# Kernel tuning notes

Hardware: AMD Instinct MI355X
Metric: run time of the kernel (lower is better)

Reference implementation:

```python
import jax, jax.numpy as jnp
import numpy as np

DELTA_V = 0.5
DELTA_D = 3.0
PARAM_VAR = 1.0
PARAM_DIST = 1.0
PARAM_REG = 0.001
NUM_BIN_LABELS = 2   # binary labels in {0,1}
NUM_INST_LABELS = 6  # background + 5 lanes


def _disc_loss_single(pred, labels, num_labels, delta_v, delta_d):
    """pred: [D, N] float, labels: [N] int in [0, num_labels).
    Assumes all labels present (true w.h.p. for large N), so
    torch.unique(sorted=True) == arange(num_labels)."""
    D, N = pred.shape
    K = num_labels
    labels = labels.astype(jnp.int32)
    ones = jnp.ones((N,), dtype=pred.dtype)
    counts = jax.ops.segment_sum(ones, labels, num_segments=K)            # [K]
    sums = jax.ops.segment_sum(pred.T, labels, num_segments=K)            # [K, D]
    means = sums / counts[:, None]                                        # [K, D] segment means

    # variance (pull) term: distance of each pixel embedding to its segment mean
    mu_expand = means[labels]                                             # [N, D]
    dist = jnp.sqrt(jnp.sum((mu_expand - pred.T) ** 2, axis=1))           # [N]
    dist = jnp.maximum(dist - delta_v, 0.0) ** 2
    var_per_label = jax.ops.segment_sum(dist, labels, num_segments=K) / counts
    l_var = jnp.mean(var_per_label)

    # distance (push) term over all ordered pairs i != j of segment means
    diff = means[:, None, :] - means[None, :, :]                          # [K, K, D]
    sq = jnp.sum(diff ** 2, axis=-1)                                      # [K, K]
    offdiag = ~jnp.eye(K, dtype=bool)
    sq_safe = jnp.where(offdiag, sq, 1.0)  # avoid sqrt(0) grad NaN on diagonal
    dn = jnp.maximum(2.0 * delta_d - jnp.sqrt(sq_safe), 0.0) ** 2
    l_dist = jnp.sum(jnp.where(offdiag, dn, 0.0)) / (K * (K - 1))

    # regularizer: mean L2 norm of segment means (norm over feature dim)
    l_reg = jnp.mean(jnp.sqrt(jnp.sum(means ** 2, axis=1)))

    return PARAM_VAR * l_var + PARAM_DIST * l_dist + PARAM_REG * l_reg


def setup_inputs() -> dict:
    key = jax.random.key(0)
    k1, k2, k3, k4 = jax.random.split(key, 4)
    B, MN = 4, 512 * 1024
    return {
        "binary_logits": jax.random.normal(k1, (B, 2, MN), dtype=jnp.float32),
        "binary_labels": jax.random.randint(k2, (B, MN), 0, NUM_BIN_LABELS, dtype=jnp.int64),
        "instance_logits": jax.random.normal(k3, (B, 5, MN), dtype=jnp.float32),
        "instance_labels": jax.random.randint(k4, (B, MN), 0, NUM_INST_LABELS, dtype=jnp.int64),
    }


def reference(binary_logits, binary_labels, instance_logits, instance_labels):
    bin_loss_per = jax.vmap(
        lambda p, l: _disc_loss_single(p, l, NUM_BIN_LABELS, DELTA_V, DELTA_D)
    )(binary_logits, binary_labels)
    inst_loss_per = jax.vmap(
        lambda p, l: _disc_loss_single(p, l, NUM_INST_LABELS, DELTA_V, DELTA_D)
    )(instance_logits, instance_labels)
    return jnp.mean(bin_loss_per), jnp.mean(inst_loss_per)
```

## Files before the change

kernel.cpp:

```cpp
#include <hip/hip_runtime.h>
#include <math.h>

#define DELTA_V 0.5f
#define DELTA_D 3.0f
#define P_REG   0.001f

#define BPS   128
#define TPB   256
#define NVMAX 36

#define P1_OFF   0
#define CNT_OFF  (8 * BPS * 36)
#define MEAN_OFF (CNT_OFF + 48)
#define LDR_OFF  (MEAN_OFF + 240)
#define P2_OFF   (LDR_OFF + 8)

template<int K, int D>
__device__ void pass1_body(const float* __restrict__ pred,
                           const int*  __restrict__ labels,
                           float* __restrict__ partials,
                           int n4, float (*lredW)[NVMAX]) {
    constexpr int NV = K * (D + 1);
    const float4* pred4 = (const float4*)pred;
    const int4*   lab4  = (const int4*)labels;

    float acc[K][D + 1];
    #pragma unroll
    for (int k = 0; k < K; ++k)
        #pragma unroll
        for (int j = 0; j <= D; ++j) acc[k][j] = 0.f;

    const int idx0   = blockIdx.x * TPB + threadIdx.x;
    const int stride = BPS * TPB;
    for (int i = idx0; i < n4; i += stride) {
        int4 lv = lab4[i];
        int labs[4] = {lv.x, lv.y, lv.z, lv.w};
        float4 xv[D];
        #pragma unroll
        for (int d = 0; d < D; ++d) xv[d] = pred4[(size_t)d * n4 + i];
        const float* xs = (const float*)&xv[0];
        #pragma unroll
        for (int c = 0; c < 4; ++c) {
            const int lab = labs[c];
            #pragma unroll
            for (int k = 0; k < K; ++k) {
                const float ind = (lab == k) ? 1.f : 0.f;
                acc[k][D] += ind;
                #pragma unroll
                for (int d = 0; d < D; ++d)
                    acc[k][d] = fmaf(ind, xs[d * 4 + c], acc[k][d]);
            }
        }
    }

    const int wave = threadIdx.x >> 6, lane = threadIdx.x & 63;
    #pragma unroll
    for (int k = 0; k < K; ++k) {
        #pragma unroll
        for (int j = 0; j <= D; ++j) {
            float v = acc[k][j];
            for (int off = 32; off > 0; off >>= 1) v += __shfl_down(v, off);
            if (lane == 0) lredW[wave][k * (D + 1) + j] = v;
        }
    }
    __syncthreads();
    if (threadIdx.x < NV) {
        const int t = threadIdx.x;
        partials[t] = lredW[0][t] + lredW[1][t] + lredW[2][t] + lredW[3][t];
    }
}

__global__ __launch_bounds__(TPB)
void pass1_fused(const float* __restrict__ bl, const int* __restrict__ bL,
                 const float* __restrict__ il, const int* __restrict__ iL,
                 float* __restrict__ ws, int MN) {
    const int s = blockIdx.y, b = s & 3;
    __shared__ float lredW[4][NVMAX];
    float* partials = ws + P1_OFF + (size_t)(s * BPS + blockIdx.x) * NVMAX;
    if (s < 4) pass1_body<2, 2>(bl + (size_t)b * 2 * MN, bL + (size_t)b * MN, partials, MN >> 2, lredW);
    else       pass1_body<6, 5>(il + (size_t)b * 5 * MN, iL + (size_t)b * MN, partials, MN >> 2, lredW);
}

__global__ void mid_kernel(float* __restrict__ ws) {
    const int s = blockIdx.x;
    const int isInst = s >> 2;
    const int K = isInst ? 6 : 2, D = isInst ? 5 : 2;
    const int NV = K * (D + 1);
    const float* P = ws + P1_OFF + (size_t)s * BPS * NVMAX;
    const int t = threadIdx.x;
    __shared__ float tot[NVMAX];
    __shared__ float muS[30];
    __shared__ float cntS[6];
    if (t < NV) {
        float v = 0.f;
        for (int j = 0; j < BPS; ++j) v += P[j * NVMAX + t];
        tot[t] = v;
        const int k = t / (D + 1), jj = t % (D + 1);
        if (jj == D) { cntS[k] = v; ws[CNT_OFF + s * 6 + k] = v; }
    }
    __syncthreads();
    if (t < NV) {
        const int k = t / (D + 1), jj = t % (D + 1);
        if (jj < D) {
            const float m = tot[t] / cntS[k];
            muS[k * D + jj] = m;
            ws[MEAN_OFF + s * 30 + k * D + jj] = m;
        }
    }
    __syncthreads();
    if (t == 0) {
        float l_dist = 0.f, l_reg = 0.f;
        for (int i = 0; i < K; ++i) {
            float n2 = 0.f;
            for (int d = 0; d < D; ++d) n2 += muS[i * D + d] * muS[i * D + d];
            l_reg += sqrtf(n2);
            for (int j = 0; j < K; ++j) {
                if (i == j) continue;
                float sq = 0.f;
                for (int d = 0; d < D; ++d) { const float df = muS[i * D + d] - muS[j * D + d]; sq += df * df; }
                const float dn = fmaxf(2.f * DELTA_D - sqrtf(sq), 0.f);
                l_dist += dn * dn;
            }
        }
        l_dist /= (float)(K * (K - 1));
        l_reg  /= (float)K;
        ws[LDR_OFF + s] = l_dist + P_REG * l_reg;
    }
}

template<int K, int D>
__device__ void pass2_body(const float* __restrict__ pred,
                           const int*  __restrict__ labels,
                           const float* __restrict__ means,
                           float* __restrict__ partials,
                           int n4, float* mu, float (*lredW)[6]) {
    if (threadIdx.x < K * D) mu[threadIdx.x] = means[threadIdx.x];
    __syncthreads();

    const float4* pred4 = (const float4*)pred;
    const int4*   lab4  = (const int4*)labels;

    float acc[K];
    #pragma unroll
    for (int k = 0; k < K; ++k) acc[k] = 0.f;

    const int idx0   = blockIdx.x * TPB + threadIdx.x;
    const int stride = BPS * TPB;
    for (int i = idx0; i < n4; i += stride) {
        int4 lv = lab4[i];
        int labs[4] = {lv.x, lv.y, lv.z, lv.w};
        float4 xv[D];
        #pragma unroll
        for (int d = 0; d < D; ++d) xv[d] = pred4[(size_t)d * n4 + i];
        const float* xs = (const float*)&xv[0];
        #pragma unroll
        for (int c = 0; c < 4; ++c) {
            const int lab = labs[c];
            float sq = 0.f;
            #pragma unroll
            for (int d = 0; d < D; ++d) {
                const float df = mu[lab * D + d] - xs[d * 4 + c];
                sq = fmaf(df, df, sq);
            }
            const float h = fmaxf(sqrtf(sq) - DELTA_V, 0.f);
            const float h2 = h * h;
            #pragma unroll
            for (int k = 0; k < K; ++k)
                acc[k] += (lab == k) ? h2 : 0.f;
        }
    }

    const int wave = threadIdx.x >> 6, lane = threadIdx.x & 63;
    #pragma unroll
    for (int k = 0; k < K; ++k) {
        float v = acc[k];
        for (int off = 32; off > 0; off >>= 1) v += __shfl_down(v, off);
        if (lane == 0) lredW[wave][k] = v;
    }
    __syncthreads();
    if (threadIdx.x < K) {
        const int t = threadIdx.x;
        partials[t] = lredW[0][t] + lredW[1][t] + lredW[2][t] + lredW[3][t];
    }
}

__global__ __launch_bounds__(TPB)
void pass2_fused(const float* __restrict__ bl, const int* __restrict__ bL,
                 const float* __restrict__ il, const int* __restrict__ iL,
                 float* __restrict__ ws, int MN) {
    const int s = blockIdx.y, b = s & 3;
    __shared__ float mu[30];
    __shared__ float lredW[4][6];
    const float* means = ws + MEAN_OFF + s * 30;
    float* partials = ws + P2_OFF + (size_t)(s * BPS + blockIdx.x) * 6;
    if (s < 4) pass2_body<2, 2>(bl + (size_t)b * 2 * MN, bL + (size_t)b * MN, means, partials, MN >> 2, mu, lredW);
    else       pass2_body<6, 5>(il + (size_t)b * 5 * MN, iL + (size_t)b * MN, means, partials, MN >> 2, mu, lredW);
}

__global__ void final_kernel(const float* __restrict__ ws, float* __restrict__ out) {
    __shared__ float contrib[48];
    const int t = threadIdx.x;
    if (t < 48) {
        const int s = t / 6, k = t % 6;
        const int Ks = (s < 4) ? 2 : 6;
        float c = 0.f;
        if (k < Ks) {
            float v = 0.f;
            for (int j = 0; j < BPS; ++j) v += ws[P2_OFF + (size_t)(s * BPS + j) * 6 + k];
            c = v / ws[CNT_OFF + s * 6 + k];
        }
        contrib[t] = c;
    }
    __syncthreads();
    if (t == 0) {
        float totB = 0.f, totI = 0.f;
        for (int s = 0; s < 8; ++s) {
            const int Ks = (s < 4) ? 2 : 6;
            float lv = 0.f;
            for (int k = 0; k < Ks; ++k) lv += contrib[s * 6 + k];
            lv /= (float)Ks;
            const float loss = lv + ws[LDR_OFF + s];
            if (s < 4) totB += loss; else totI += loss;
        }
        out[0] = totB * 0.25f;
        out[1] = totI * 0.25f;
    }
}

extern "C" void kernel_launch(void* const* d_in, const int* in_sizes, int n_in,
                              void* d_out, int out_size, void* d_ws, size_t ws_size,
                              hipStream_t stream) {
    const float* bin_logits  = (const float*)d_in[0];
    const int*   bin_labels  = (const int*)d_in[1];
    const float* inst_logits = (const float*)d_in[2];
    const int*   inst_labels = (const int*)d_in[3];
    float* ws  = (float*)d_ws;
    float* out = (float*)d_out;

    const int B  = 4;
    const int MN = in_sizes[1] / B;

    dim3 grid(BPS, 8), block(TPB);
    pass1_fused<<<grid, block, 0, stream>>>(bin_logits, bin_labels, inst_logits, inst_labels, ws, MN);
    mid_kernel<<<8, 64, 0, stream>>>(ws);
    pass2_fused<<<grid, block, 0, stream>>>(bin_logits, bin_labels, inst_logits, inst_labels, ws, MN);
    final_kernel<<<1, 64, 0, stream>>>(ws, out);
}
```

Measured before the change: 141.0 us.

## Fuse all passes into one cooperative kernel keeping inputs in registers

```diff
diff --git a/kernel.cpp b/kernel.cpp
--- a/kernel.cpp
+++ b/kernel.cpp
@@ -1,16 +1,259 @@
 #include <hip/hip_runtime.h>
+#include <hip/hip_cooperative_groups.h>
 #include <math.h>
+
+namespace cg = cooperative_groups;
 
 #define DELTA_V 0.5f
 #define DELTA_D 3.0f
 #define P_REG   0.001f
-
-#define BPS   128
-#define TPB   256
-#define NVMAX 36
-
+#define TPB     256
+#define NVMAX   36
+
+typedef float f32x4 __attribute__((ext_vector_type(4)));
+typedef int   i32x4 __attribute__((ext_vector_type(4)));
+
+#define BPSB 64
+#define BPSI 128
+#define NBLK (4 * BPSB + 4 * BPSI)
+
+#define FP1_OFF   0
+#define FCNT_OFF  (NBLK * NVMAX)
+#define FMEAN_OFF (FCNT_OFF + 48)
+#define FLDR_OFF  (FMEAN_OFF + 240)
+#define FP2_OFF   (FLDR_OFF + 8)
+
+__device__ __forceinline__ int slice_block_base(int s) {
+    return (s < 4) ? s * BPSB : 4 * BPSB + (s - 4) * BPSI;
+}
+
+template<int K, int D, int NBP>
+__device__ void reduce_means(const float* __restrict__ ws, int sliceBase,
+                             float* cntS, float* muS) {
+    constexpr int NV = K * (D + 1);
+    constexpr int G  = TPB / NV;
+    __shared__ float red[TPB];
+    __shared__ float tot[NVMAX];
+    const int t = threadIdx.x;
+    if (t < G * NV) {
+        const int g = t / NV, v = t - g * NV;
+        float sm = 0.f;
+        for (int j = g; j < NBP; j += G)
+            sm += ws[FP1_OFF + (size_t)(sliceBase + j) * NVMAX + v];
+        red[t] = sm;
+    }
+    __syncthreads();
+    if (t < NV) {
+        float sm = 0.f;
+        #pragma unroll
+        for (int g = 0; g < G; ++g) sm += red[g * NV + t];
+        tot[t] = sm;
+        const int k = t / (D + 1), jj = t - k * (D + 1);
+        if (jj == D) cntS[k] = sm;
+    }
+    __syncthreads();
+    if (t < NV) {
+        const int k = t / (D + 1), jj = t - k * (D + 1);
+        if (jj < D) muS[k * D + jj] = tot[t] / cntS[k];
+    }
+    __syncthreads();
+}
+
+__device__ void final_body(const float* __restrict__ ws, float* __restrict__ out) {
+    __shared__ float contrib[48];
+    const int t = threadIdx.x;
+    if (t < 48) {
+        const int s = t / 6, k = t - s * 6;
+        const int Ks = (s < 4) ? 2 : 6;
+        const int NB = (s < 4) ? BPSB : BPSI;
+        const int base = slice_block_base(s);
+        float c = 0.f;
+        if (k < Ks) {
+            float v = 0.f;
+            for (int j = 0; j < NB; ++j)
+                v += ws[FP2_OFF + (size_t)(base + j) * 6 + k];
+            c = v / ws[FCNT_OFF + s * 6 + k];
+        }
+        contrib[t] = c;
+    }
+    __syncthreads();
+    if (t == 0) {
+        float totB = 0.f, totI = 0.f;
+        for (int s = 0; s < 8; ++s) {
+            const int Ks = (s < 4) ? 2 : 6;
+            float lv = 0.f;
+            for (int k = 0; k < Ks; ++k) lv += contrib[s * 6 + k];
+            lv /= (float)Ks;
+            const float loss = lv + ws[FLDR_OFF + s];
+            if (s < 4) totB += loss; else totI += loss;
+        }
+        out[0] = totB * 0.25f;
+        out[1] = totI * 0.25f;
+    }
+}
+
+template<int K, int D, int NITER, int NBP>
+__device__ void run_slice(const float* __restrict__ pred, const int* __restrict__ labels,
+                          float* __restrict__ ws, float* __restrict__ out,
+                          const int s, const int bx, const int bid, const int n4) {
+    constexpr int NV = K * (D + 1);
+    const f32x4* __restrict__ pred4 = (const f32x4*)pred;
+    const i32x4* __restrict__ lab4  = (const i32x4*)labels;
+
+    __shared__ float lredW[4][NVMAX];
+    __shared__ float cntS[6];
+    __shared__ float muS[30];
+
+    f32x4 xv[NITER][D];
+    int   lp[NITER];
+
+    const int idx0 = bx * TPB + threadIdx.x;
+    const f32x4 zero4 = {0.f, 0.f, 0.f, 0.f};
+
+    #pragma unroll
+    for (int it = 0; it < NITER; ++it) {
+        const int i = idx0 + it * (NBP * TPB);
+        if (i < n4) {
+            const i32x4 l4 = lab4[i];
+            lp[it] = l4[0] | (l4[1] << 8) | (l4[2] << 16) | (l4[3] << 24);
+            #pragma unroll
+            for (int d = 0; d < D; ++d) xv[it][d] = pred4[(size_t)d * n4 + i];
+        } else {
+            lp[it] = -1;
+            #pragma unroll
+            for (int d = 0; d < D; ++d) xv[it][d] = zero4;
+        }
+    }
+
+    float acc[K][D + 1];
+    #pragma unroll
+    for (int k = 0; k < K; ++k) {
+        #pragma unroll
+        for (int j = 0; j <= D; ++j) acc[k][j] = 0.f;
+    }
+    #pragma unroll
+    for (int it = 0; it < NITER; ++it) {
+        #pragma unroll
+        for (int c = 0; c < 4; ++c) {
+            const int lab = (lp[it] >> (8 * c)) & 0xFF;
+            #pragma unroll
+            for (int k = 0; k < K; ++k) {
+                const float ind = (lab == k) ? 1.f : 0.f;
+                acc[k][D] += ind;
+                #pragma unroll
+                for (int d = 0; d < D; ++d)
+                    acc[k][d] = fmaf(ind, xv[it][d][c], acc[k][d]);
+            }
+        }
+    }
+
+    const int wave = threadIdx.x >> 6, lane = threadIdx.x & 63;
+    #pragma unroll
+    for (int k = 0; k < K; ++k) {
+        #pragma unroll
+        for (int j = 0; j <= D; ++j) {
+            float v = acc[k][j];
+            #pragma unroll
+            for (int off = 32; off; off >>= 1) v += __shfl_down(v, off);
+            if (lane == 0) lredW[wave][k * (D + 1) + j] = v;
+        }
+    }
+    __syncthreads();
+    if (threadIdx.x < NV)
+        ws[FP1_OFF + (size_t)bid * NVMAX + threadIdx.x] =
+            lredW[0][threadIdx.x] + lredW[1][threadIdx.x] +
+            lredW[2][threadIdx.x] + lredW[3][threadIdx.x];
+
+    cg::grid_group grid = cg::this_grid();
+    grid.sync();
+
+    reduce_means<K, D, NBP>(ws, bid - bx, cntS, muS);
+
+    if (bx == 0) {
+        const int t = threadIdx.x;
+        if (t < K) ws[FCNT_OFF + s * 6 + t] = cntS[t];
+        if (t < K * D) ws[FMEAN_OFF + s * 30 + t] = muS[t];
+        if (t == 0) {
+            float l_dist = 0.f, l_reg = 0.f;
+            for (int i = 0; i < K; ++i) {
+                float n2 = 0.f;
+                for (int d = 0; d < D; ++d) n2 += muS[i * D + d] * muS[i * D + d];
+                l_reg += sqrtf(n2);
+                for (int j = 0; j < K; ++j) {
+                    if (i == j) continue;
+                    float sq = 0.f;
+                    for (int d = 0; d < D; ++d) {
+                        const float df = muS[i * D + d] - muS[j * D + d];
+                        sq += df * df;
+                    }
+                    const float dn = fmaxf(2.f * DELTA_D - sqrtf(sq), 0.f);
+                    l_dist += dn * dn;
+                }
+            }
+            ws[FLDR_OFF + s] = l_dist / (float)(K * (K - 1)) + P_REG * (l_reg / (float)K);
+        }
+    }
+
+    float acc2[K];
+    #pragma unroll
+    for (int k = 0; k < K; ++k) acc2[k] = 0.f;
+    #pragma unroll
+    for (int it = 0; it < NITER; ++it) {
+        #pragma unroll
+        for (int c = 0; c < 4; ++c) {
+            const int lab = (lp[it] >> (8 * c)) & 0xFF;
+            const int lb  = (lab < K) ? lab : 0;
+            float sq = 0.f;
+            #pragma unroll
+            for (int d = 0; d < D; ++d) {
+                const float df = muS[lb * D + d] - xv[it][d][c];
+                sq = fmaf(df, df, sq);
+            }
+            const float h  = fmaxf(sqrtf(sq) - DELTA_V, 0.f);
+            const float h2 = h * h;
+            #pragma unroll
+            for (int k = 0; k < K; ++k) acc2[k] += (lab == k) ? h2 : 0.f;
+        }
+    }
+    #pragma unroll
+    for (int k = 0; k < K; ++k) {
+        float v = acc2[k];
+        #pragma unroll
+        for (int off = 32; off; off >>= 1) v += __shfl_down(v, off);
+        if (lane == 0) lredW[wave][k] = v;
+    }
+    __syncthreads();
+    if (threadIdx.x < K)
+        ws[FP2_OFF + (size_t)bid * 6 + threadIdx.x] =
+            lredW[0][threadIdx.x] + lredW[1][threadIdx.x] +
+            lredW[2][threadIdx.x] + lredW[3][threadIdx.x];
+
+    grid.sync();
+
+    if (bid == 0) final_body(ws, out);
+}
+
+__global__ __launch_bounds__(TPB, 3)
+void fused_kernel(const float* __restrict__ bl, const int* __restrict__ bL,
+                  const float* __restrict__ il, const int* __restrict__ iL,
+                  float* __restrict__ ws, float* __restrict__ out, int MN) {
+    const int bid = blockIdx.x;
+    const int n4  = MN >> 2;
+    if (bid < 4 * BPSB) {
+        const int s = bid / BPSB, bx = bid - s * BPSB;
+        run_slice<2, 2, 8, BPSB>(bl + (size_t)s * 2 * MN, bL + (size_t)s * MN,
+                                 ws, out, s, bx, bid, n4);
+    } else {
+        const int r = bid - 4 * BPSB;
+        const int si = r / BPSI, bx = r - si * BPSI;
+        run_slice<6, 5, 4, BPSI>(il + (size_t)si * 5 * MN, iL + (size_t)si * MN,
+                                 ws, out, 4 + si, bx, bid, n4);
+    }
+}
+
+#define OBPS 128
 #define P1_OFF   0
-#define CNT_OFF  (8 * BPS * 36)
+#define CNT_OFF  (8 * OBPS * 36)
 #define MEAN_OFF (CNT_OFF + 48)
 #define LDR_OFF  (MEAN_OFF + 240)
 #define P2_OFF   (LDR_OFF + 8)
@@ -26,19 +269,20 @@
 
     float acc[K][D + 1];
     #pragma unroll
-    for (int k = 0; k < K; ++k)
+    for (int k = 0; k < K; ++k) {
         #pragma unroll
         for (int j = 0; j <= D; ++j) acc[k][j] = 0.f;
+    }
 
     const int idx0   = blockIdx.x * TPB + threadIdx.x;
-    const int stride = BPS * TPB;
+    const int stride = OBPS * TPB;
     for (int i = idx0; i < n4; i += stride) {
         int4 lv = lab4[i];
         int labs[4] = {lv.x, lv.y, lv.z, lv.w};
-        float4 xv[D];
-        #pragma unroll
-        for (int d = 0; d < D; ++d) xv[d] = pred4[(size_t)d * n4 + i];
-        const float* xs = (const float*)&xv[0];
+        float4 xvv[D];
+        #pragma unroll
+        for (int d = 0; d < D; ++d) xvv[d] = pred4[(size_t)d * n4 + i];
+        const float* xs = (const float*)&xvv[0];
         #pragma unroll
         for (int c = 0; c < 4; ++c) {
             const int lab = labs[c];
@@ -76,7 +320,7 @@
                  float* __restrict__ ws, int MN) {
     const int s = blockIdx.y, b = s & 3;
     __shared__ float lredW[4][NVMAX];
-    float* partials = ws + P1_OFF + (size_t)(s * BPS + blockIdx.x) * NVMAX;
+    float* partials = ws + P1_OFF + (size_t)(s * OBPS + blockIdx.x) * NVMAX;
     if (s < 4) pass1_body<2, 2>(bl + (size_t)b * 2 * MN, bL + (size_t)b * MN, partials, MN >> 2, lredW);
     else       pass1_body<6, 5>(il + (size_t)b * 5 * MN, iL + (size_t)b * MN, partials, MN >> 2, lredW);
 }
@@ -86,14 +330,14 @@
     const int isInst = s >> 2;
     const int K = isInst ? 6 : 2, D = isInst ? 5 : 2;
     const int NV = K * (D + 1);
-    const float* P = ws + P1_OFF + (size_t)s * BPS * NVMAX;
+    const float* P = ws + P1_OFF + (size_t)s * OBPS * NVMAX;
     const int t = threadIdx.x;
     __shared__ float tot[NVMAX];
     __shared__ float muS[30];
     __shared__ float cntS[6];
     if (t < NV) {
         float v = 0.f;
-        for (int j = 0; j < BPS; ++j) v += P[j * NVMAX + t];
+        for (int j = 0; j < OBPS; ++j) v += P[j * NVMAX + t];
         tot[t] = v;
         const int k = t / (D + 1), jj = t % (D + 1);
         if (jj == D) { cntS[k] = v; ws[CNT_OFF + s * 6 + k] = v; }
@@ -145,14 +389,14 @@
     for (int k = 0; k < K; ++k) acc[k] = 0.f;
 
     const int idx0   = blockIdx.x * TPB + threadIdx.x;
-    const int stride = BPS * TPB;
+    const int stride = OBPS * TPB;
     for (int i = idx0; i < n4; i += stride) {
         int4 lv = lab4[i];
         int labs[4] = {lv.x, lv.y, lv.z, lv.w};
-        float4 xv[D];
-        #pragma unroll
-        for (int d = 0; d < D; ++d) xv[d] = pred4[(size_t)d * n4 + i];
-        const float* xs = (const float*)&xv[0];
+        float4 xvv[D];
+        #pragma unroll
+        for (int d = 0; d < D; ++d) xvv[d] = pred4[(size_t)d * n4 + i];
+        const float* xs = (const float*)&xvv[0];
         #pragma unroll
         for (int c = 0; c < 4; ++c) {
             const int lab = labs[c];
@@ -192,7 +436,7 @@
     __shared__ float mu[30];
     __shared__ float lredW[4][6];
     const float* means = ws + MEAN_OFF + s * 30;
-    float* partials = ws + P2_OFF + (size_t)(s * BPS + blockIdx.x) * 6;
+    float* partials = ws + P2_OFF + (size_t)(s * OBPS + blockIdx.x) * 6;
     if (s < 4) pass2_body<2, 2>(bl + (size_t)b * 2 * MN, bL + (size_t)b * MN, means, partials, MN >> 2, mu, lredW);
     else       pass2_body<6, 5>(il + (size_t)b * 5 * MN, iL + (size_t)b * MN, means, partials, MN >> 2, mu, lredW);
 }
@@ -206,7 +450,7 @@
         float c = 0.f;
         if (k < Ks) {
             float v = 0.f;
-            for (int j = 0; j < BPS; ++j) v += ws[P2_OFF + (size_t)(s * BPS + j) * 6 + k];
+            for (int j = 0; j < OBPS; ++j) v += ws[P2_OFF + (size_t)(s * OBPS + j) * 6 + k];
             c = v / ws[CNT_OFF + s * 6 + k];
         }
         contrib[t] = c;
@@ -230,19 +474,28 @@
 extern "C" void kernel_launch(void* const* d_in, const int* in_sizes, int n_in,
                               void* d_out, int out_size, void* d_ws, size_t ws_size,
                               hipStream_t stream) {
-    const float* bin_logits  = (const float*)d_in[0];
-    const int*   bin_labels  = (const int*)d_in[1];
-    const float* inst_logits = (const float*)d_in[2];
-    const int*   inst_labels = (const int*)d_in[3];
+    const float* bl = (const float*)d_in[0];
+    const int*   bL = (const int*)d_in[1];
+    const float* il = (const float*)d_in[2];
+    const int*   iL = (const int*)d_in[3];
     float* ws  = (float*)d_ws;
     float* out = (float*)d_out;
 
     const int B  = 4;
-    const int MN = in_sizes[1] / B;
-
-    dim3 grid(BPS, 8), block(TPB);
-    pass1_fused<<<grid, block, 0, stream>>>(bin_logits, bin_labels, inst_logits, inst_labels, ws, MN);
-    mid_kernel<<<8, 64, 0, stream>>>(ws);
-    pass2_fused<<<grid, block, 0, stream>>>(bin_logits, bin_labels, inst_logits, inst_labels, ws, MN);
-    final_kernel<<<1, 64, 0, stream>>>(ws, out);
-}
+    int MN = in_sizes[1] / B;
+
+    void* args[] = {(void*)&bl, (void*)&bL, (void*)&il, (void*)&iL,
+                    (void*)&ws, (void*)&out, (void*)&MN};
+    hipError_t err = hipLaunchCooperativeKernel(
+        reinterpret_cast<const void*>(&fused_kernel),
+        dim3(NBLK), dim3(TPB), args, 0u, stream);
+
+    if (err != hipSuccess) {
+        (void)hipGetLastError();
+        dim3 grid(OBPS, 8), block(TPB);
+        pass1_fused<<<grid, block, 0, stream>>>(bl, bL, il, iL, ws, MN);
+        mid_kernel<<<8, 64, 0, stream>>>(ws);
+        pass2_fused<<<grid, block, 0, stream>>>(bl, bL, il, iL, ws, MN);
+        final_kernel<<<1, 64, 0, stream>>>(ws, out);
+    }
+}
```

Result: slower. 269.3 us (+90.9%).

## Fold mid and final kernels into pass2, rebalance blocks toward instance slices

Applied to the files above, without the earlier changes.

```diff
diff --git a/kernel.cpp b/kernel.cpp
--- a/kernel.cpp
+++ b/kernel.cpp
@@ -4,22 +4,28 @@
 #define DELTA_V 0.5f
 #define DELTA_D 3.0f
 #define P_REG   0.001f
-
-#define BPS   128
-#define TPB   256
-#define NVMAX 36
-
-#define P1_OFF   0
-#define CNT_OFF  (8 * BPS * 36)
-#define MEAN_OFF (CNT_OFF + 48)
-#define LDR_OFF  (MEAN_OFF + 240)
-#define P2_OFF   (LDR_OFF + 8)
+#define TPB     256
+#define NVMAX   36
+
+#define BPSB 128
+#define BPSI 256
+#define NBLK (4 * BPSB + 4 * BPSI)
+
+#define CTR_OFF   0
+#define P1_OFF    16
+#define SCAL_OFF  (P1_OFF + NBLK * NVMAX)
+#define P2_OFF    (SCAL_OFF + 64)
+
+__device__ __forceinline__ int slice_base(int s) {
+    return (s < 4) ? s * BPSB : 4 * BPSB + (s - 4) * BPSI;
+}
 
 template<int K, int D>
 __device__ void pass1_body(const float* __restrict__ pred,
                            const int*  __restrict__ labels,
                            float* __restrict__ partials,
-                           int n4, float (*lredW)[NVMAX]) {
+                           int n4, int bx, int stride,
+                           float (*lredW)[NVMAX]) {
     constexpr int NV = K * (D + 1);
     const float4* pred4 = (const float4*)pred;
     const int4*   lab4  = (const int4*)labels;
@@ -30,8 +36,7 @@
         #pragma unroll
         for (int j = 0; j <= D; ++j) acc[k][j] = 0.f;
 
-    const int idx0   = blockIdx.x * TPB + threadIdx.x;
-    const int stride = BPS * TPB;
+    const int idx0 = bx * TPB + threadIdx.x;
     for (int i = idx0; i < n4; i += stride) {
         int4 lv = lab4[i];
         int labs[4] = {lv.x, lv.y, lv.z, lv.w};
@@ -71,71 +76,111 @@
 }
 
 __global__ __launch_bounds__(TPB)
-void pass1_fused(const float* __restrict__ bl, const int* __restrict__ bL,
-                 const float* __restrict__ il, const int* __restrict__ iL,
-                 float* __restrict__ ws, int MN) {
-    const int s = blockIdx.y, b = s & 3;
+void pass1_k(const float* __restrict__ bl, const int* __restrict__ bL,
+             const float* __restrict__ il, const int* __restrict__ iL,
+             float* __restrict__ ws, int MN) {
+    if (blockIdx.x == 0 && threadIdx.x == 0) ((int*)ws)[CTR_OFF] = 0;
+
     __shared__ float lredW[4][NVMAX];
-    float* partials = ws + P1_OFF + (size_t)(s * BPS + blockIdx.x) * NVMAX;
-    if (s < 4) pass1_body<2, 2>(bl + (size_t)b * 2 * MN, bL + (size_t)b * MN, partials, MN >> 2, lredW);
-    else       pass1_body<6, 5>(il + (size_t)b * 5 * MN, iL + (size_t)b * MN, partials, MN >> 2, lredW);
-}
-
-__global__ void mid_kernel(float* __restrict__ ws) {
-    const int s = blockIdx.x;
-    const int isInst = s >> 2;
-    const int K = isInst ? 6 : 2, D = isInst ? 5 : 2;
-    const int NV = K * (D + 1);
-    const float* P = ws + P1_OFF + (size_t)s * BPS * NVMAX;
+    const int bid = blockIdx.x, n4 = MN >> 2;
+    float* partials = ws + P1_OFF + (size_t)bid * NVMAX;
+    if (bid < 4 * BPSB) {
+        const int s = bid / BPSB, bx = bid - s * BPSB;
+        pass1_body<2, 2>(bl + (size_t)s * 2 * MN, bL + (size_t)s * MN,
+                         partials, n4, bx, BPSB * TPB, lredW);
+    } else {
+        const int r = bid - 4 * BPSB;
+        const int si = r / BPSI, bx = r - si * BPSI;
+        pass1_body<6, 5>(il + (size_t)si * 5 * MN, iL + (size_t)si * MN,
+                         partials, n4, bx, BPSI * TPB, lredW);
+    }
+}
+
+__device__ void final_body(const float* __restrict__ ws, float* __restrict__ out) {
+    __shared__ float contrib[48];
     const int t = threadIdx.x;
+    if (t < 48) {
+        const int s = t / 6, k = t - (t / 6) * 6;
+        const int Ks = (s < 4) ? 2 : 6;
+        const int NB = (s < 4) ? BPSB : BPSI;
+        const int base = slice_base(s);
+        float c = 0.f;
+        if (k < Ks) {
+            float v = 0.f;
+            for (int j = 0; j < NB; ++j)
+                v += ws[P2_OFF + (size_t)(base + j) * 6 + k];
+            c = v / ws[SCAL_OFF + s * 8 + k];
+        }
+        contrib[t] = c;
+    }
+    __syncthreads();
+    if (t == 0) {
+        float totB = 0.f, totI = 0.f;
+        for (int s = 0; s < 8; ++s) {
+            const int Ks = (s < 4) ? 2 : 6;
+            float lv = 0.f;
+            for (int k = 0; k < Ks; ++k) lv += contrib[s * 6 + k];
+            lv /= (float)Ks;
+            const float loss = lv + ws[SCAL_OFF + s * 8 + 6];
+            if (s < 4) totB += loss; else totI += loss;
+        }
+        out[0] = totB * 0.25f;
+        out[1] = totI * 0.25f;
+    }
+}
+
+template<int K, int D, int NBP>
+__device__ void pass2_slice(const float* __restrict__ pred,
+                            const int*  __restrict__ labels,
+                            float* __restrict__ ws, float* __restrict__ out,
+                            const int s, const int bx, const int bid, const int n4) {
+    constexpr int NV = K * (D + 1);
     __shared__ float tot[NVMAX];
     __shared__ float muS[30];
     __shared__ float cntS[6];
+    __shared__ float lredW[4][6];
+    __shared__ int lastFlag;
+    const int t = threadIdx.x;
+    const int sliceBase = bid - bx;
+
     if (t < NV) {
+        const float* P = ws + P1_OFF + (size_t)sliceBase * NVMAX + t;
         float v = 0.f;
-        for (int j = 0; j < BPS; ++j) v += P[j * NVMAX + t];
+        for (int j = 0; j < NBP; ++j) v += P[(size_t)j * NVMAX];
         tot[t] = v;
-        const int k = t / (D + 1), jj = t % (D + 1);
-        if (jj == D) { cntS[k] = v; ws[CNT_OFF + s * 6 + k] = v; }
+        const int k = t / (D + 1), jj = t - k * (D + 1);
+        if (jj == D) cntS[k] = v;
     }
     __syncthreads();
     if (t < NV) {
-        const int k = t / (D + 1), jj = t % (D + 1);
-        if (jj < D) {
-            const float m = tot[t] / cntS[k];
-            muS[k * D + jj] = m;
-            ws[MEAN_OFF + s * 30 + k * D + jj] = m;
-        }
-    }
-    __syncthreads();
-    if (t == 0) {
-        float l_dist = 0.f, l_reg = 0.f;
-        for (int i = 0; i < K; ++i) {
-            float n2 = 0.f;
-            for (int d = 0; d < D; ++d) n2 += muS[i * D + d] * muS[i * D + d];
-            l_reg += sqrtf(n2);
-            for (int j = 0; j < K; ++j) {
-                if (i == j) continue;
-                float sq = 0.f;
-                for (int d = 0; d < D; ++d) { const float df = muS[i * D + d] - muS[j * D + d]; sq += df * df; }
-                const float dn = fmaxf(2.f * DELTA_D - sqrtf(sq), 0.f);
-                l_dist += dn * dn;
+        const int k = t / (D + 1), jj = t - k * (D + 1);
+        if (jj < D) muS[k * D + jj] = tot[t] / cntS[k];
+    }
+    __syncthreads();
+
+    if (bx == 0) {
+        if (t < K) ws[SCAL_OFF + s * 8 + t] = cntS[t];
+        if (t == 0) {
+            float l_dist = 0.f, l_reg = 0.f;
+            for (int i = 0; i < K; ++i) {
+                float n2 = 0.f;
+                for (int d = 0; d < D; ++d) n2 += muS[i * D + d] * muS[i * D + d];
+                l_reg += sqrtf(n2);
+                for (int j = 0; j < K; ++j) {
+                    if (i == j) continue;
+                    float sq = 0.f;
+                    for (int d = 0; d < D; ++d) {
+                        const float df = muS[i * D + d] - muS[j * D + d];
+                        sq += df * df;
+                    }
+                    const float dn = fmaxf(2.f * DELTA_D - sqrtf(sq), 0.f);
+                    l_dist += dn * dn;
+                }
             }
-        }
-        l_dist /= (float)(K * (K - 1));
-        l_reg  /= (float)K;
-        ws[LDR_OFF + s] = l_dist + P_REG * l_reg;
-    }
-}
-
-template<int K, int D>
-__device__ void pass2_body(const float* __restrict__ pred,
-                           const int*  __restrict__ labels,
-                           const float* __restrict__ means,
-                           float* __restrict__ partials,
-                           int n4, float* mu, float (*lredW)[6]) {
-    if (threadIdx.x < K * D) mu[threadIdx.x] = means[threadIdx.x];
-    __syncthreads();
+            ws[SCAL_OFF + s * 8 + 6] =
+                l_dist / (float)(K * (K - 1)) + P_REG * (l_reg / (float)K);
+        }
+    }
 
     const float4* pred4 = (const float4*)pred;
     const int4*   lab4  = (const int4*)labels;
@@ -144,8 +189,8 @@
     #pragma unroll
     for (int k = 0; k < K; ++k) acc[k] = 0.f;
 
-    const int idx0   = blockIdx.x * TPB + threadIdx.x;
-    const int stride = BPS * TPB;
+    const int idx0 = bx * TPB + t;
+    const int stride = NBP * TPB;
     for (int i = idx0; i < n4; i += stride) {
         int4 lv = lab4[i];
         int labs[4] = {lv.x, lv.y, lv.z, lv.w};
@@ -159,7 +204,7 @@
             float sq = 0.f;
             #pragma unroll
             for (int d = 0; d < D; ++d) {
-                const float df = mu[lab * D + d] - xs[d * 4 + c];
+                const float df = muS[lab * D + d] - xs[d * 4 + c];
                 sq = fmaf(df, df, sq);
             }
             const float h = fmaxf(sqrtf(sq) - DELTA_V, 0.f);
@@ -170,7 +215,7 @@
         }
     }
 
-    const int wave = threadIdx.x >> 6, lane = threadIdx.x & 63;
+    const int wave = t >> 6, lane = t & 63;
     #pragma unroll
     for (int k = 0; k < K; ++k) {
         float v = acc[k];
@@ -178,71 +223,55 @@
         if (lane == 0) lredW[wave][k] = v;
     }
     __syncthreads();
-    if (threadIdx.x < K) {
-        const int t = threadIdx.x;
-        partials[t] = lredW[0][t] + lredW[1][t] + lredW[2][t] + lredW[3][t];
+    if (t < K)
+        ws[P2_OFF + (size_t)bid * 6 + t] =
+            lredW[0][t] + lredW[1][t] + lredW[2][t] + lredW[3][t];
+
+    __syncthreads();
+    if (t == 0) {
+        __threadfence();
+        const int old = __hip_atomic_fetch_add((int*)ws + CTR_OFF, 1,
+                                               __ATOMIC_ACQ_REL,
+                                               __HIP_MEMORY_SCOPE_AGENT);
+        lastFlag = (old == NBLK - 1);
+    }
+    __syncthreads();
+    if (lastFlag) {
+        __threadfence();
+        final_body(ws, out);
     }
 }
 
 __global__ __launch_bounds__(TPB)
-void pass2_fused(const float* __restrict__ bl, const int* __restrict__ bL,
-                 const float* __restrict__ il, const int* __restrict__ iL,
-                 float* __restrict__ ws, int MN) {
-    const int s = blockIdx.y, b = s & 3;
-    __shared__ float mu[30];
-    __shared__ float lredW[4][6];
-    const float* means = ws + MEAN_OFF + s * 30;
-    float* partials = ws + P2_OFF + (size_t)(s * BPS + blockIdx.x) * 6;
-    if (s < 4) pass2_body<2, 2>(bl + (size_t)b * 2 * MN, bL + (size_t)b * MN, means, partials, MN >> 2, mu, lredW);
-    else       pass2_body<6, 5>(il + (size_t)b * 5 * MN, iL + (size_t)b * MN, means, partials, MN >> 2, mu, lredW);
-}
-
-__global__ void final_kernel(const float* __restrict__ ws, float* __restrict__ out) {
-    __shared__ float contrib[48];
-    const int t = threadIdx.x;
-    if (t < 48) {
-        const int s = t / 6, k = t % 6;
-        const int Ks = (s < 4) ? 2 : 6;
-        float c = 0.f;
-        if (k < Ks) {
-            float v = 0.f;
-            for (int j = 0; j < BPS; ++j) v += ws[P2_OFF + (size_t)(s * BPS + j) * 6 + k];
-            c = v / ws[CNT_OFF + s * 6 + k];
-        }
-        contrib[t] = c;
-    }
-    __syncthreads();
-    if (t == 0) {
-        float totB = 0.f, totI = 0.f;
-        for (int s = 0; s < 8; ++s) {
-            const int Ks = (s < 4) ? 2 : 6;
-            float lv = 0.f;
-            for (int k = 0; k < Ks; ++k) lv += contrib[s * 6 + k];
-            lv /= (float)Ks;
-            const float loss = lv + ws[LDR_OFF + s];
-            if (s < 4) totB += loss; else totI += loss;
-        }
-        out[0] = totB * 0.25f;
-        out[1] = totI * 0.25f;
+void pass2_k(const float* __restrict__ bl, const int* __restrict__ bL,
+             const float* __restrict__ il, const int* __restrict__ iL,
+             float* __restrict__ ws, float* __restrict__ out, int MN) {
+    const int bid = blockIdx.x, n4 = MN >> 2;
+    if (bid < 4 * BPSB) {
+        const int s = bid / BPSB, bx = bid - s * BPSB;
+        pass2_slice<2, 2, BPSB>(bl + (size_t)s * 2 * MN, bL + (size_t)s * MN,
+                                ws, out, s, bx, bid, n4);
+    } else {
+        const int r = bid - 4 * BPSB;
+        const int si = r / BPSI, bx = r - si * BPSI;
+        pass2_slice<6, 5, BPSI>(il + (size_t)si * 5 * MN, iL + (size_t)si * MN,
+                                ws, out, 4 + si, bx, bid, n4);
     }
 }
 
 extern "C" void kernel_launch(void* const* d_in, const int* in_sizes, int n_in,
                               void* d_out, int out_size, void* d_ws, size_t ws_size,
                               hipStream_t stream) {
-    const float* bin_logits  = (const float*)d_in[0];
-    const int*   bin_labels  = (const int*)d_in[1];
-    const float* inst_logits = (const float*)d_in[2];
-    const int*   inst_labels = (const int*)d_in[3];
+    const float* bl = (const float*)d_in[0];
+    const int*   bL = (const int*)d_in[1];
+    const float* il = (const float*)d_in[2];
+    const int*   iL = (const int*)d_in[3];
     float* ws  = (float*)d_ws;
     float* out = (float*)d_out;
 
     const int B  = 4;
     const int MN = in_sizes[1] / B;
 
-    dim3 grid(BPS, 8), block(TPB);
-    pass1_fused<<<grid, block, 0, stream>>>(bin_logits, bin_labels, inst_logits, inst_labels, ws, MN);
-    mid_kernel<<<8, 64, 0, stream>>>(ws);
-    pass2_fused<<<grid, block, 0, stream>>>(bin_logits, bin_labels, inst_logits, inst_labels, ws, MN);
-    final_kernel<<<1, 64, 0, stream>>>(ws, out);
-}
+    pass1_k<<<dim3(NBLK), dim3(TPB), 0, stream>>>(bl, bL, il, iL, ws, MN);
+    pass2_k<<<dim3(NBLK), dim3(TPB), 0, stream>>>(bl, bL, il, iL, ws, out, MN);
+}
```

Measured after the change: 225.0 us. +59.6%, slower.
